# Optimization experiments

Hardware: AMD Instinct MI355X
Metric: run time of the kernel (lower is better)

The kernel has to match this reference:

```python
import jax, jax.numpy as jnp
import numpy as np

IN_FEATURES = 512
OUT_FEATURES = 512
INIT_SCALE = 0.05


def setup_inputs() -> dict:
    key = jax.random.key(0)
    kx, kw = jax.random.split(key)
    x = jax.random.normal(kx, (2048, IN_FEATURES), dtype=jnp.float32)
    W = jax.random.normal(kw, (OUT_FEATURES, IN_FEATURES), dtype=jnp.float32) * INIT_SCALE
    return {"x": x, "W": W}


def reference(x, W):
    # Tropical (max-plus) matmul: y[b, i] = max_j (W[i, j] + x[b, j])
    # Broadcast-add builds the (B, out, in) intermediate, then max-reduce over in,
    # exactly matching the torch module's eval-mode path (T=None, training=False).
    sums = x[:, None, :] + W[None, :, :]  # (B, out, in)
    return jnp.max(sums, axis=-1)         # (B, out)
```

## Files before the change

### kernel.cpp

```cpp
#include <hip/hip_runtime.h>
#include <math.h>


#define B_ROWS 2048
#define K_DIM  512
#define O_DIM  512

#define WS_WT_OFF 256
#define WS_NEED_BYTES ((size_t)(WS_WT_OFF + K_DIM * O_DIM) * sizeof(float))

__global__ __launch_bounds__(256) void prep_transpose_minmax(
    const float* __restrict__ W, float* __restrict__ ws)
{
    __shared__ float sm[64][65];
    __shared__ float wmin[4], wmax[4];

    const int t  = threadIdx.x;
    const int bx = blockIdx.x;
    const int tr = (bx >> 3) * 64;
    const int tc = (bx & 7) * 64;

    const int lr0 = t >> 4;
    const int lc  = (t & 15) * 4;

    float lmin = INFINITY, lmax = -INFINITY;
#pragma unroll
    for (int q = 0; q < 4; ++q) {
        const int r = lr0 + q * 16;
        float4 v = *(const float4*)(W + (size_t)(tr + r) * K_DIM + tc + lc);
        sm[r][lc + 0] = v.x; sm[r][lc + 1] = v.y;
        sm[r][lc + 2] = v.z; sm[r][lc + 3] = v.w;
        lmin = fminf(lmin, fminf(fminf(v.x, v.y), fminf(v.z, v.w)));
        lmax = fmaxf(lmax, fmaxf(fmaxf(v.x, v.y), fmaxf(v.z, v.w)));
    }
    __syncthreads();

    float* Wt = ws + WS_WT_OFF;
#pragma unroll
    for (int q = 0; q < 4; ++q) {
        const int kr = lr0 + q * 16;
        float4 v;
        v.x = sm[lc + 0][kr]; v.y = sm[lc + 1][kr];
        v.z = sm[lc + 2][kr]; v.w = sm[lc + 3][kr];
        *(float4*)(Wt + (size_t)(tc + kr) * O_DIM + tr + lc) = v;
    }

#pragma unroll
    for (int off = 32; off; off >>= 1) {
        lmin = fminf(lmin, __shfl_xor(lmin, off));
        lmax = fmaxf(lmax, __shfl_xor(lmax, off));
    }
    if ((t & 63) == 0) { wmin[t >> 6] = lmin; wmax[t >> 6] = lmax; }
    __syncthreads();
    if (t == 0) {
        ws[2 * bx]     = fminf(fminf(wmin[0], wmin[1]), fminf(wmin[2], wmin[3]));
        ws[2 * bx + 1] = fmaxf(fmaxf(wmax[0], wmax[1]), fmaxf(wmax[2], wmax[3]));
    }
}

__global__ __launch_bounds__(256) void tropical_sparse(
    const float* __restrict__ x, const float* __restrict__ ws,
    float* __restrict__ out)
{
    const int t    = threadIdx.x;
    const int w    = t >> 6;
    const int lane = t & 63;
    const int b    = blockIdx.x * 4 + w;
    const float* Wt = ws + WS_WT_OFF;

    const float* xr = x + (size_t)b * K_DIM + lane * 8;
    float4 xa = *(const float4*)(xr);
    float4 xb = *(const float4*)(xr + 4);
    float xs[8] = {xa.x, xa.y, xa.z, xa.w, xb.x, xb.y, xb.z, xb.w};

    float bmin = ws[2 * lane], bmax = ws[2 * lane + 1];
#pragma unroll
    for (int off = 32; off; off >>= 1) {
        bmin = fminf(bmin, __shfl_xor(bmin, off));
        bmax = fmaxf(bmax, __shfl_xor(bmax, off));
    }
    const float dW = bmax - bmin;

    float m = xs[0];
#pragma unroll
    for (int i = 1; i < 8; ++i) m = fmaxf(m, xs[i]);
#pragma unroll
    for (int off = 32; off; off >>= 1) m = fmaxf(m, __shfl_xor(m, off));
    const float thr = m - dW;

    float acc[8];
#pragma unroll
    for (int i = 0; i < 8; ++i) acc[i] = -INFINITY;

    const int o0 = lane * 8;
#pragma unroll
    for (int s = 0; s < 8; ++s) {
        unsigned long long mask = __ballot(xs[s] >= thr);
        while (mask) {
            const int src = __ffsll((unsigned long long)mask) - 1;
            mask &= mask - 1;
            const float xv = __shfl(xs[s], src);
            const int k = src * 8 + s;
            const float* wr = Wt + (size_t)k * O_DIM + o0;
            float4 wa = *(const float4*)(wr);
            float4 wb = *(const float4*)(wr + 4);
            acc[0] = fmaxf(acc[0], xv + wa.x);
            acc[1] = fmaxf(acc[1], xv + wa.y);
            acc[2] = fmaxf(acc[2], xv + wa.z);
            acc[3] = fmaxf(acc[3], xv + wa.w);
            acc[4] = fmaxf(acc[4], xv + wb.x);
            acc[5] = fmaxf(acc[5], xv + wb.y);
            acc[6] = fmaxf(acc[6], xv + wb.z);
            acc[7] = fmaxf(acc[7], xv + wb.w);
        }
    }

    float* op = out + (size_t)b * O_DIM + o0;
    float4 r0, r1;
    r0.x = acc[0]; r0.y = acc[1]; r0.z = acc[2]; r0.w = acc[3];
    r1.x = acc[4]; r1.y = acc[5]; r1.z = acc[6]; r1.w = acc[7];
    *(float4*)(op)     = r0;
    *(float4*)(op + 4) = r1;
}

__global__ __launch_bounds__(256) void tropical_naive(
    const float* __restrict__ x, const float* __restrict__ W,
    float* __restrict__ out)
{
    const int b = blockIdx.x;
    const int t = threadIdx.x;
#pragma unroll
    for (int half = 0; half < 2; ++half) {
        const int o = t + half * 256;
        const float* wr = W + (size_t)o * K_DIM;
        const float* xr = x + (size_t)b * K_DIM;
        float acc = -INFINITY;
        for (int k = 0; k < K_DIM; ++k)
            acc = fmaxf(acc, xr[k] + wr[k]);
        out[(size_t)b * O_DIM + o] = acc;
    }
}

extern "C" void kernel_launch(void* const* d_in, const int* in_sizes, int n_in,
                              void* d_out, int out_size, void* d_ws, size_t ws_size,
                              hipStream_t stream) {
    const float* x = (const float*)d_in[0];
    const float* W = (const float*)d_in[1];
    float* out = (float*)d_out;

    if (ws_size >= WS_NEED_BYTES) {
        prep_transpose_minmax<<<64, 256, 0, stream>>>(W, (float*)d_ws);
        tropical_sparse<<<B_ROWS / 4, 256, 0, stream>>>(
            x, (const float*)d_ws, out);
    } else {
        tropical_naive<<<B_ROWS, 256, 0, stream>>>(x, W, out);
    }
}
```

Measured before the change: 65.28 us.

## Fuse W transpose/minmax prep into sparse kernel with atomic flag barrier

Measured after the change: 133.6 us. 2.05x slower.

```diff
diff --git a/kernel.cpp b/kernel.cpp
--- a/kernel.cpp
+++ b/kernel.cpp
@@ -6,98 +6,104 @@
 #define K_DIM  512
 #define O_DIM  512
 
-#define WS_WT_OFF 256
-#define WS_NEED_BYTES ((size_t)(WS_WT_OFF + K_DIM * O_DIM) * sizeof(float))
+#define WS_PAIRS 2
+#define WS_WT    2304
+#define WS_NEED_BYTES ((size_t)(WS_WT + K_DIM * O_DIM) * sizeof(float))
+#define NWORK 64u
 
-__global__ __launch_bounds__(256) void prep_transpose_minmax(
-    const float* __restrict__ W, float* __restrict__ ws)
+__global__ __launch_bounds__(256) void tropical_fused(
+    const float* __restrict__ x, const float* __restrict__ W,
+    float* __restrict__ ws, float* __restrict__ out)
 {
     __shared__ float sm[64][65];
-    __shared__ float wmin[4], wmax[4];
+    __shared__ float wmin4[4], wmax4[4];
 
     const int t  = threadIdx.x;
     const int bx = blockIdx.x;
-    const int tr = (bx >> 3) * 64;
-    const int tc = (bx & 7) * 64;
+    unsigned int* flag = (unsigned int*)ws;
+    float* Wt = ws + WS_WT;
 
-    const int lr0 = t >> 4;
-    const int lc  = (t & 15) * 4;
+    if (bx < 64) {
+        const int tr  = (bx >> 3) * 64;
+        const int tc  = (bx & 7) * 64;
+        const int lr0 = t >> 4;
+        const int lc  = (t & 15) * 4;
 
-    float lmin = INFINITY, lmax = -INFINITY;
+        float lmin = INFINITY, lmax = -INFINITY;
 #pragma unroll
-    for (int q = 0; q < 4; ++q) {
-        const int r = lr0 + q * 16;
-        float4 v = *(const float4*)(W + (size_t)(tr + r) * K_DIM + tc + lc);
-        sm[r][lc + 0] = v.x; sm[r][lc + 1] = v.y;
-        sm[r][lc + 2] = v.z; sm[r][lc + 3] = v.w;
-        lmin = fminf(lmin, fminf(fminf(v.x, v.y), fminf(v.z, v.w)));
-        lmax = fmaxf(lmax, fmaxf(fmaxf(v.x, v.y), fmaxf(v.z, v.w)));
-    }
-    __syncthreads();
-
-    float* Wt = ws + WS_WT_OFF;
+        for (int q = 0; q < 4; ++q) {
+            const int r = lr0 + q * 16;
+            float4 v = *(const float4*)(W + (size_t)(tr + r) * K_DIM + tc + lc);
+            sm[r][lc + 0] = v.x; sm[r][lc + 1] = v.y;
+            sm[r][lc + 2] = v.z; sm[r][lc + 3] = v.w;
+            lmin = fminf(lmin, fminf(fminf(v.x, v.y), fminf(v.z, v.w)));
+            lmax = fmaxf(lmax, fmaxf(fmaxf(v.x, v.y), fmaxf(v.z, v.w)));
+        }
+        __syncthreads();
 #pragma unroll
-    for (int q = 0; q < 4; ++q) {
-        const int kr = lr0 + q * 16;
-        float4 v;
-        v.x = sm[lc + 0][kr]; v.y = sm[lc + 1][kr];
-        v.z = sm[lc + 2][kr]; v.w = sm[lc + 3][kr];
-        *(float4*)(Wt + (size_t)(tc + kr) * O_DIM + tr + lc) = v;
+        for (int q = 0; q < 4; ++q) {
+            const int kr = lr0 + q * 16;
+            float4 v;
+            v.x = sm[lc + 0][kr]; v.y = sm[lc + 1][kr];
+            v.z = sm[lc + 2][kr]; v.w = sm[lc + 3][kr];
+            *(float4*)(Wt + (size_t)(tc + kr) * O_DIM + tr + lc) = v;
+        }
+#pragma unroll
+        for (int off = 32; off; off >>= 1) {
+            lmin = fminf(lmin, __shfl_xor(lmin, off));
+            lmax = fmaxf(lmax, __shfl_xor(lmax, off));
+        }
+        if ((t & 63) == 0) { wmin4[t >> 6] = lmin; wmax4[t >> 6] = lmax; }
+        __syncthreads();
+        if (t == 0) {
+            ws[WS_PAIRS + 2 * bx] =
+                fminf(fminf(wmin4[0], wmin4[1]), fminf(wmin4[2], wmin4[3]));
+            ws[WS_PAIRS + 2 * bx + 1] =
+                fmaxf(fmaxf(wmax4[0], wmax4[1]), fmaxf(wmax4[2], wmax4[3]));
+        }
+        __threadfence();
+        __syncthreads();
+        if (t == 0)
+            __hip_atomic_fetch_add(flag, 1u, __ATOMIC_RELEASE,
+                                   __HIP_MEMORY_SCOPE_AGENT);
     }
 
-#pragma unroll
-    for (int off = 32; off; off >>= 1) {
-        lmin = fminf(lmin, __shfl_xor(lmin, off));
-        lmax = fmaxf(lmax, __shfl_xor(lmax, off));
-    }
-    if ((t & 63) == 0) { wmin[t >> 6] = lmin; wmax[t >> 6] = lmax; }
-    __syncthreads();
-    if (t == 0) {
-        ws[2 * bx]     = fminf(fminf(wmin[0], wmin[1]), fminf(wmin[2], wmin[3]));
-        ws[2 * bx + 1] = fmaxf(fmaxf(wmax[0], wmax[1]), fmaxf(wmax[2], wmax[3]));
-    }
-}
-
-__global__ __launch_bounds__(256) void tropical_sparse(
-    const float* __restrict__ x, const float* __restrict__ ws,
-    float* __restrict__ out)
-{
-    const int t    = threadIdx.x;
     const int w    = t >> 6;
     const int lane = t & 63;
-    const int b    = blockIdx.x * 4 + w;
-    const float* Wt = ws + WS_WT_OFF;
-
+    const int b    = bx * 4 + w;
     const float* xr = x + (size_t)b * K_DIM + lane * 8;
     float4 xa = *(const float4*)(xr);
     float4 xb = *(const float4*)(xr + 4);
     float xs[8] = {xa.x, xa.y, xa.z, xa.w, xb.x, xb.y, xb.z, xb.w};
+    float m = xs[0];
+#pragma unroll
+    for (int i = 1; i < 8; ++i) m = fmaxf(m, xs[i]);
+#pragma unroll
+    for (int off = 32; off; off >>= 1) m = fmaxf(m, __shfl_xor(m, off));
 
-    float bmin = ws[2 * lane], bmax = ws[2 * lane + 1];
+    while (__hip_atomic_load(flag, __ATOMIC_ACQUIRE,
+                             __HIP_MEMORY_SCOPE_AGENT) < NWORK)
+        __builtin_amdgcn_s_sleep(2);
+
+    float bmin = ws[WS_PAIRS + 2 * lane];
+    float bmax = ws[WS_PAIRS + 2 * lane + 1];
 #pragma unroll
     for (int off = 32; off; off >>= 1) {
         bmin = fminf(bmin, __shfl_xor(bmin, off));
         bmax = fmaxf(bmax, __shfl_xor(bmax, off));
     }
-    const float dW = bmax - bmin;
-
-    float m = xs[0];
-#pragma unroll
-    for (int i = 1; i < 8; ++i) m = fmaxf(m, xs[i]);
-#pragma unroll
-    for (int off = 32; off; off >>= 1) m = fmaxf(m, __shfl_xor(m, off));
-    const float thr = m - dW;
+    const float thr = m - (bmax - bmin);
 
     float acc[8];
 #pragma unroll
     for (int i = 0; i < 8; ++i) acc[i] = -INFINITY;
+    const int o0 = lane * 8;
 
-    const int o0 = lane * 8;
 #pragma unroll
     for (int s = 0; s < 8; ++s) {
         unsigned long long mask = __ballot(xs[s] >= thr);
         while (mask) {
-            const int src = __ffsll((unsigned long long)mask) - 1;
+            const int src = __ffsll(mask) - 1;
             mask &= mask - 1;
             const float xv = __shfl(xs[s], src);
             const int k = src * 8 + s;
@@ -116,11 +122,8 @@
     }
 
     float* op = out + (size_t)b * O_DIM + o0;
-    float4 r0, r1;
-    r0.x = acc[0]; r0.y = acc[1]; r0.z = acc[2]; r0.w = acc[3];
-    r1.x = acc[4]; r1.y = acc[5]; r1.z = acc[6]; r1.w = acc[7];
-    *(float4*)(op)     = r0;
-    *(float4*)(op + 4) = r1;
+    *(float4*)(op)     = make_float4(acc[0], acc[1], acc[2], acc[3]);
+    *(float4*)(op + 4) = make_float4(acc[4], acc[5], acc[6], acc[7]);
 }
 
 __global__ __launch_bounds__(256) void tropical_naive(
@@ -149,9 +152,9 @@
     float* out = (float*)d_out;
 
     if (ws_size >= WS_NEED_BYTES) {
-        prep_transpose_minmax<<<64, 256, 0, stream>>>(W, (float*)d_ws);
-        tropical_sparse<<<B_ROWS / 4, 256, 0, stream>>>(
-            x, (const float*)d_ws, out);
+        hipMemsetAsync(d_ws, 0, 4, stream);
+        tropical_fused<<<512, 256, 0, stream>>>(
+            x, W, (float*)d_ws, out);
     } else {
         tropical_naive<<<B_ROWS, 256, 0, stream>>>(x, W, out);
     }
```
